# Performance work log

Hardware: AMD Instinct MI355X
Metric: run time of the kernel (lower is better)

Reference implementation:

```python
import jax, jax.numpy as jnp
import numpy as np

B, S, D, H = 2, 4096, 256, 8
P = 64               # proj_dim_l
R = S // P           # proj_dim_r = 64, P*R == S
DH = D // H          # head_dim = 32


def setup_inputs() -> dict:
    key = jax.random.key(0)
    kx, kl, kr, kv, ko = jax.random.split(key, 5)
    scale = 0.05  # stand-in for xavier-uniform scale
    x  = jax.random.normal(kx, (B, S, D), dtype=jnp.float32)
    Wl = jax.random.normal(kl, (D, P), dtype=jnp.float32) * scale
    Wr = jax.random.normal(kr, (D, R), dtype=jnp.float32) * scale
    Wv = jax.random.normal(kv, (D, D), dtype=jnp.float32) * scale
    Wo = jax.random.normal(ko, (D, D), dtype=jnp.float32) * scale
    return {"x": x, "Wl": Wl, "Wr": Wr, "Wv": Wv, "Wo": Wo}


def reference(x, Wl, Wr, Wv, Wo):
    b, s, d = x.shape
    # value projection + head split -> (b, H, S, DH). Dropout p=0 (eval) = identity.
    v = (x @ Wv).reshape(b, s, H, DH).transpose(0, 2, 1, 3)
    # factorized score: row n is vec(outer(l_n, r_n)) of length P*R == S
    l = x @ Wl                                   # (b, S, P)
    r = x @ Wr                                   # (b, S, R)
    attn = (l[:, :, :, None] * r[:, :, None, :]).reshape(b, s, s)  # (b, S, S)
    score = jax.nn.softmax(attn, axis=-1)        # (b, S, S)
    # shared score across heads, per-head value matmul
    o = jnp.einsum('bnm,bhmd->bhnd', score, v)   # (b, H, S, DH)
    o = o.transpose(0, 2, 1, 3).reshape(b, s, d) # concat heads
    return o @ Wo
```

## Files before the change

kernel.cpp:

```cpp
#include <hip/hip_runtime.h>
#include <hip/hip_bf16.h>

typedef __attribute__((ext_vector_type(8))) __bf16 bf16x8;
typedef __attribute__((ext_vector_type(4))) __bf16 bf16x4;
typedef __attribute__((ext_vector_type(4))) float  f32x4;

#define MFMA16(a, b, c) __builtin_amdgcn_mfma_f32_16x16x32_bf16((a), (b), (c), 0, 0, 0)

static constexpr size_t OFF_WVT  = 0;
static constexpr size_t OFF_WLT  = OFF_WVT + 256 * 256 * 2;
static constexpr size_t OFF_WRT  = OFF_WLT + 64 * 256 * 2;
static constexpr size_t OFF_WOT  = OFF_WRT + 64 * 256 * 2;
static constexpr size_t OFF_VT   = 1u << 20;
static constexpr size_t OFF_L    = 6u << 20;
static constexpr size_t OFF_R    = 8u << 20;
static constexpr size_t OFF_PART = 10u << 20;
static constexpr size_t OFF_ZP   = 26u << 20;

__device__ __forceinline__ float fast_exp2(float x) {
  float e;
  asm("v_exp_f32 %0, %1" : "=v"(e) : "v"(x));
  return e;
}

__device__ __forceinline__ bf16x8 cvt8(float4 a, float4 b) {
  bf16x8 o;
  o[0] = (__bf16)a.x; o[1] = (__bf16)a.y; o[2] = (__bf16)a.z; o[3] = (__bf16)a.w;
  o[4] = (__bf16)b.x; o[5] = (__bf16)b.y; o[6] = (__bf16)b.z; o[7] = (__bf16)b.w;
  return o;
}

__global__ __launch_bounds__(256) void k_prepw(const float* __restrict__ Wv,
                                               const float* __restrict__ Wl,
                                               const float* __restrict__ Wr,
                                               const float* __restrict__ Wo,
                                               __bf16* __restrict__ Wvt,
                                               __bf16* __restrict__ Wlt,
                                               __bf16* __restrict__ Wrt,
                                               __bf16* __restrict__ Wot) {
  const int idx = blockIdx.x * 256 + threadIdx.x;
  if (idx < 65536) {
    const int k = idx >> 8, n = idx & 255;
    Wvt[n * 256 + k] = (__bf16)Wv[idx];
  } else if (idx < 81920) {
    const int j = idx - 65536;
    const int k = j >> 6, n = j & 63;
    Wlt[n * 256 + k] = (__bf16)Wl[j];
  } else if (idx < 98304) {
    const int j = idx - 81920;
    const int k = j >> 6, n = j & 63;
    Wrt[n * 256 + k] = (__bf16)Wr[j];
  } else {
    const int j = idx - 98304;
    const int k = j >> 8, n = j & 255;
    Wot[n * 256 + k] = (__bf16)Wo[j];
  }
}

__global__ __launch_bounds__(256) void k_proj(const float* __restrict__ x,
                                              const __bf16* __restrict__ Wvt,
                                              const __bf16* __restrict__ Wlt,
                                              const __bf16* __restrict__ Wrt,
                                              __bf16* __restrict__ Vt,
                                              float* __restrict__ lbuf,
                                              float* __restrict__ rbuf) {
  __shared__ __align__(16) __bf16 vs[8 * 64 * 8];
  const int t = threadIdx.x;
  const int lane = t & 63, wave = t >> 6;
  const int l16 = lane & 15, quad = lane >> 4;
  const int wr = wave >> 1, wc = wave & 1;
  const int rbk = blockIdx.x;
  const int ct  = blockIdx.y;
  const __bf16* Wt;
  int colbase;
  if (ct < 4)       { Wt = Wvt; colbase = ct * 64; }
  else if (ct == 4) { Wt = Wlt; colbase = 0; }
  else              { Wt = Wrt; colbase = 0; }
  const int row0 = rbk * 64 + wr * 32;
  const int c0   = colbase + wc * 32;
  f32x4 acc[2][2] = {};
  for (int kk = 0; kk < 256; kk += 32) {
    const int ko = kk + quad * 8;
    const float* xr0 = x + (size_t)(row0 + l16) * 256 + ko;
    const float* xr1 = x + (size_t)(row0 + 16 + l16) * 256 + ko;
    bf16x8 a0 = cvt8(*(const float4*)xr0, *(const float4*)(xr0 + 4));
    bf16x8 a1 = cvt8(*(const float4*)xr1, *(const float4*)(xr1 + 4));
    bf16x8 b0 = *(const bf16x8*)(Wt + (size_t)(c0 + l16) * 256 + ko);
    bf16x8 b1 = *(const bf16x8*)(Wt + (size_t)(c0 + 16 + l16) * 256 + ko);
    acc[0][0] = MFMA16(a0, b0, acc[0][0]);
    acc[0][1] = MFMA16(a0, b1, acc[0][1]);
    acc[1][0] = MFMA16(a1, b0, acc[1][0]);
    acc[1][1] = MFMA16(a1, b1, acc[1][1]);
  }
  if (ct < 4) {
#pragma unroll
    for (int mt = 0; mt < 2; ++mt)
#pragma unroll
      for (int nt = 0; nt < 2; ++nt) {
        const int m8 = wr * 4 + mt * 2 + (quad >> 1);
        const int d  = wc * 32 + nt * 16 + l16;
        bf16x4 o;
        o.x = (__bf16)acc[mt][nt][0];
        o.y = (__bf16)acc[mt][nt][1];
        o.z = (__bf16)acc[mt][nt][2];
        o.w = (__bf16)acc[mt][nt][3];
        *(bf16x4*)(&vs[m8 * 512 + d * 8 + (quad & 1) * 4]) = o;
      }
    __syncthreads();
    const int m8 = t >> 5, s32 = t & 31;
    const int bat = rbk >> 6, mc = rbk & 63;
    bf16x8 a = *(const bf16x8*)(&vs[m8 * 512 + s32 * 16]);
    bf16x8 b = *(const bf16x8*)(&vs[m8 * 512 + s32 * 16 + 8]);
    __bf16* dst = Vt + (size_t)bat * 1048576 + (size_t)mc * 16384 +
                  m8 * 2048 + ct * 512 + s32 * 16;
    *(bf16x8*)dst       = a;
    *(bf16x8*)(dst + 8) = b;
  } else {
    float* dstb = (ct == 4) ? lbuf : rbuf;
#pragma unroll
    for (int mt = 0; mt < 2; ++mt)
#pragma unroll
      for (int nt = 0; nt < 2; ++nt) {
        const int col = c0 + nt * 16 + l16;
        const int gr  = rbk * 64 + wr * 32 + mt * 16 + quad * 4;
#pragma unroll
        for (int rr = 0; rr < 4; ++rr)
          dstb[(size_t)(gr + rr) * 64 + col] = acc[mt][nt][rr];
      }
  }
}

__global__ __launch_bounds__(512, 2) void k_attn(const float* __restrict__ lbuf,
                                                 const float* __restrict__ rbuf,
                                                 const __bf16* __restrict__ Vt,
                                                 __bf16* __restrict__ part,
                                                 float* __restrict__ zpart) {
  __shared__ __align__(16) char smem[74240];
  __bf16* vt0 = (__bf16*)smem;
  __bf16* vt1 = (__bf16*)(smem + 32768);
  float*  ls  = (float*)(smem + 65536);
  const int t = threadIdx.x;
  const int lane = t & 63, w = t >> 6;
  const int l16 = lane & 15, quad = lane >> 4;
  const int wr = w >> 1, wc = w & 1;
  const int rb = blockIdx.x;
  const int sp = blockIdx.y;
  const int g0 = rb * 128;
  const int bat = rb >> 5;
  const __bf16* Vbase = Vt + (size_t)bat * 1048576;
  const int ck0 = sp * 16;

  {
    const int idx = t * 4;
    const int row = idx >> 4, c = idx & 15;
    f32x4 v = *(const f32x4*)(lbuf + (size_t)(g0 + row) * 64 + ck0 + c);
    ls[row * 17 + c + 0] = v[0];
    ls[row * 17 + c + 1] = v[1];
    ls[row * 17 + c + 2] = v[2];
    ls[row * 17 + c + 3] = v[3];
  }
  const float LOG2E = 1.44269504088896f;
  float rreg[2][16];
#pragma unroll
  for (int mt = 0; mt < 2; ++mt) {
    const float* rp = rbuf + (size_t)(g0 + wr * 32 + mt * 16 + l16) * 64;
    f32x4 a = *(const f32x4*)(rp + quad * 8);
    f32x4 b = *(const f32x4*)(rp + quad * 8 + 4);
    f32x4 c = *(const f32x4*)(rp + 32 + quad * 8);
    f32x4 d = *(const f32x4*)(rp + 32 + quad * 8 + 4);
#pragma unroll
    for (int j = 0; j < 4; ++j) {
      rreg[mt][j]      = a[j] * LOG2E;
      rreg[mt][4 + j]  = b[j] * LOG2E;
      rreg[mt][8 + j]  = c[j] * LOG2E;
      rreg[mt][12 + j] = d[j] * LOG2E;
    }
  }

  f32x4 acc[2][8] = {};
  float zacc[2] = {0.f, 0.f};
  bf16x8 stg[4];

  {
    const __bf16* src = Vbase + (size_t)ck0 * 16384;
#pragma unroll
    for (int i = 0; i < 4; ++i) stg[i] = *(const bf16x8*)(src + (size_t)(i * 512 + t) * 8);
#pragma unroll
    for (int i = 0; i < 4; ++i) *(bf16x8*)(vt0 + (i * 512 + t) * 8) = stg[i];
  }
  __syncthreads();

  for (int kc = 0; kc < 16; ++kc) {
    __bf16* cur = (kc & 1) ? vt1 : vt0;
    __bf16* nxt = (kc & 1) ? vt0 : vt1;
    if (kc < 15) {
      const __bf16* src = Vbase + (size_t)(ck0 + kc + 1) * 16384;
#pragma unroll
      for (int i = 0; i < 4; ++i) stg[i] = *(const bf16x8*)(src + (size_t)(i * 512 + t) * 8);
    }
    bf16x8 af[2][2];
#pragma unroll
    for (int mt = 0; mt < 2; ++mt) {
      const float lv = ls[(wr * 32 + mt * 16 + l16) * 17 + kc];
#pragma unroll
      for (int kk = 0; kk < 2; ++kk)
#pragma unroll
        for (int j = 0; j < 8; ++j) {
          const float e = fast_exp2(lv * rreg[mt][kk * 8 + j]);
          zacc[mt] += e;
          af[mt][kk][j] = (__bf16)e;
        }
    }
#pragma unroll
    for (int kk = 0; kk < 2; ++kk)
#pragma unroll
      for (int nt = 0; nt < 8; ++nt) {
        bf16x8 bv = *(const bf16x8*)(cur + (kk * 4 + quad) * 2048 +
                                     (wc * 128 + nt * 16 + l16) * 8);
        acc[0][nt] = MFMA16(af[0][kk], bv, acc[0][nt]);
        acc[1][nt] = MFMA16(af[1][kk], bv, acc[1][nt]);
      }
    if (kc < 15) {
#pragma unroll
      for (int i = 0; i < 4; ++i) *(bf16x8*)(nxt + (i * 512 + t) * 8) = stg[i];
    }
    __syncthreads();
  }

#pragma unroll
  for (int mt = 0; mt < 2; ++mt) {
    float z = zacc[mt];
    z += __shfl_xor(z, 16);
    z += __shfl_xor(z, 32);
    if (wc == 0 && quad == 0)
      zpart[(size_t)sp * 8192 + g0 + wr * 32 + mt * 16 + l16] = z;
  }

  __bf16* ctile = (__bf16*)smem;
#pragma unroll
  for (int mt = 0; mt < 2; ++mt)
#pragma unroll
    for (int nt = 0; nt < 8; ++nt) {
      const int r0 = wr * 32 + mt * 16 + quad * 4;
      const int c  = wc * 128 + nt * 16 + l16;
#pragma unroll
      for (int rr = 0; rr < 4; ++rr)
        ctile[(r0 + rr) * 264 + c] = (__bf16)acc[mt][nt][rr];
    }
  __syncthreads();
  __bf16* pb = part + (size_t)sp * (8192 * 256);
#pragma unroll
  for (int p = 0; p < 8; ++p) {
    const int u = p * 512 + t;
    const int row = u >> 5, seg = u & 31;
    *(bf16x8*)(pb + (size_t)(g0 + row) * 256 + seg * 8) =
        *(const bf16x8*)(ctile + row * 264 + seg * 8);
  }
}

__global__ __launch_bounds__(256) void k_outfix(const __bf16* __restrict__ part,
                                                const float* __restrict__ zpart,
                                                const __bf16* __restrict__ Wot,
                                                float* __restrict__ out) {
  const int t = threadIdx.x;
  const int lane = t & 63, w = t >> 6;
  const int l16 = lane & 15, quad = lane >> 4;
  const int wr = w >> 1, wc = w & 1;
  const int rb = blockIdx.x;
  const int arow = rb * 32 + wr * 16 + l16;
  float z = 0.f;
#pragma unroll
  for (int s = 0; s < 4; ++s) z += zpart[(size_t)s * 8192 + arow];
  const float iz = 1.0f / z;
  f32x4 acc[8] = {};
#pragma unroll 2
  for (int ks = 0; ks < 8; ++ks) {
    const int k0 = ks * 32 + quad * 8;
    float sum[8] = {};
#pragma unroll
    for (int s = 0; s < 4; ++s) {
      bf16x8 p = *(const bf16x8*)(part + (size_t)s * (8192 * 256) + (size_t)arow * 256 + k0);
#pragma unroll
      for (int j = 0; j < 8; ++j) sum[j] += (float)p[j];
    }
    bf16x8 afr;
#pragma unroll
    for (int j = 0; j < 8; ++j) afr[j] = (__bf16)(sum[j] * iz);
#pragma unroll
    for (int nt = 0; nt < 8; ++nt) {
      bf16x8 bv = *(const bf16x8*)(Wot + (size_t)(wc * 128 + nt * 16 + l16) * 256 + k0);
      acc[nt] = MFMA16(afr, bv, acc[nt]);
    }
  }
#pragma unroll
  for (int nt = 0; nt < 8; ++nt) {
    const int col = wc * 128 + nt * 16 + l16;
    const int r0  = rb * 32 + wr * 16 + quad * 4;
#pragma unroll
    for (int rr = 0; rr < 4; ++rr)
      out[(size_t)(r0 + rr) * 256 + col] = acc[nt][rr];
  }
}

extern "C" void kernel_launch(void* const* d_in, const int* in_sizes, int n_in,
                              void* d_out, int out_size, void* d_ws, size_t ws_size,
                              hipStream_t stream) {
  const float* x  = (const float*)d_in[0];
  const float* Wl = (const float*)d_in[1];
  const float* Wr = (const float*)d_in[2];
  const float* Wv = (const float*)d_in[3];
  const float* Wo = (const float*)d_in[4];
  char* ws = (char*)d_ws;
  __bf16* Wvt = (__bf16*)(ws + OFF_WVT);
  __bf16* Wlt = (__bf16*)(ws + OFF_WLT);
  __bf16* Wrt = (__bf16*)(ws + OFF_WRT);
  __bf16* Wot = (__bf16*)(ws + OFF_WOT);
  __bf16* Vt  = (__bf16*)(ws + OFF_VT);
  float*  lb  = (float*)(ws + OFF_L);
  float*  rbf = (float*)(ws + OFF_R);
  __bf16* prt = (__bf16*)(ws + OFF_PART);
  float*  zp  = (float*)(ws + OFF_ZP);
  float*  out = (float*)d_out;

  k_prepw<<<640, 256, 0, stream>>>(Wv, Wl, Wr, Wo, Wvt, Wlt, Wrt, Wot);
  k_proj<<<dim3(128, 6), 256, 0, stream>>>(x, Wvt, Wlt, Wrt, Vt, lb, rbf);
  k_attn<<<dim3(64, 4), 512, 0, stream>>>(lb, rbf, Vt, prt, zp);
  k_outfix<<<256, 256, 0, stream>>>(prt, zp, Wot, out);
}
```

Before: 135.2 us.

## Fold Wo into Wv weights and stage V tiles with direct global-to-LDS loads

Precomputes Wv·Wo in the weight-prep kernel, using the fact that the per-head value and output projections are linear and the shared softmax commutes with them. The final kernel then becomes a simple normalize-and-sum of partials, with no MFMA output GEMM. The attention kernel's V double-buffer now uses global_load_lds instead of register staging followed by LDS stores. The folded weight product runs as a scalar fp32 loop in prep, and the fused weights are quantized to bf16 once, which changes rounding.

```diff
diff --git a/kernel.cpp b/kernel.cpp
--- a/kernel.cpp
+++ b/kernel.cpp
@@ -10,7 +10,6 @@
 static constexpr size_t OFF_WVT  = 0;
 static constexpr size_t OFF_WLT  = OFF_WVT + 256 * 256 * 2;
 static constexpr size_t OFF_WRT  = OFF_WLT + 64 * 256 * 2;
-static constexpr size_t OFF_WOT  = OFF_WRT + 64 * 256 * 2;
 static constexpr size_t OFF_VT   = 1u << 20;
 static constexpr size_t OFF_L    = 6u << 20;
 static constexpr size_t OFF_R    = 8u << 20;
@@ -28,6 +27,12 @@
   o[0] = (__bf16)a.x; o[1] = (__bf16)a.y; o[2] = (__bf16)a.z; o[3] = (__bf16)a.w;
   o[4] = (__bf16)b.x; o[5] = (__bf16)b.y; o[6] = (__bf16)b.z; o[7] = (__bf16)b.w;
   return o;
+}
+
+__device__ __forceinline__ void gll16(const __bf16* g, __bf16* l) {
+  __builtin_amdgcn_global_load_lds((const __attribute__((address_space(1))) void*)g,
+                                   (__attribute__((address_space(3))) void*)l,
+                                   16, 0, 0);
 }
 
 __global__ __launch_bounds__(256) void k_prepw(const float* __restrict__ Wv,
@@ -36,24 +41,32 @@
                                                const float* __restrict__ Wo,
                                                __bf16* __restrict__ Wvt,
                                                __bf16* __restrict__ Wlt,
-                                               __bf16* __restrict__ Wrt,
-                                               __bf16* __restrict__ Wot) {
-  const int idx = blockIdx.x * 256 + threadIdx.x;
-  if (idx < 65536) {
-    const int k = idx >> 8, n = idx & 255;
-    Wvt[n * 256 + k] = (__bf16)Wv[idx];
-  } else if (idx < 81920) {
-    const int j = idx - 65536;
-    const int k = j >> 6, n = j & 63;
-    Wlt[n * 256 + k] = (__bf16)Wl[j];
-  } else if (idx < 98304) {
-    const int j = idx - 81920;
-    const int k = j >> 6, n = j & 63;
-    Wrt[n * 256 + k] = (__bf16)Wr[j];
+                                               __bf16* __restrict__ Wrt) {
+  const int blk = blockIdx.x;
+  const int t = threadIdx.x;
+  if (blk < 128) {
+    const int idx = blk * 256 + t;
+    if (idx < 16384) {
+      const int k = idx >> 6, n = idx & 63;
+      Wlt[n * 256 + k] = (__bf16)Wl[idx];
+    } else {
+      const int j = idx - 16384;
+      const int k = j >> 6, n = j & 63;
+      Wrt[n * 256 + k] = (__bf16)Wr[j];
+    }
   } else {
-    const int j = idx - 98304;
-    const int k = j >> 8, n = j & 255;
-    Wot[n * 256 + k] = (__bf16)Wo[j];
+    const int k = blk - 128;
+    const int n = t;
+    const float* wvr = Wv + (size_t)k * 256;
+    float a0 = 0.f, a1 = 0.f, a2 = 0.f, a3 = 0.f;
+#pragma unroll 4
+    for (int j = 0; j < 256; j += 4) {
+      a0 += wvr[j + 0] * Wo[(size_t)(j + 0) * 256 + n];
+      a1 += wvr[j + 1] * Wo[(size_t)(j + 1) * 256 + n];
+      a2 += wvr[j + 2] * Wo[(size_t)(j + 2) * 256 + n];
+      a3 += wvr[j + 3] * Wo[(size_t)(j + 3) * 256 + n];
+    }
+    Wvt[(size_t)n * 256 + k] = (__bf16)((a0 + a1) + (a2 + a3));
   }
 }
 
@@ -179,14 +192,12 @@
 
   f32x4 acc[2][8] = {};
   float zacc[2] = {0.f, 0.f};
-  bf16x8 stg[4];
 
   {
     const __bf16* src = Vbase + (size_t)ck0 * 16384;
 #pragma unroll
-    for (int i = 0; i < 4; ++i) stg[i] = *(const bf16x8*)(src + (size_t)(i * 512 + t) * 8);
-#pragma unroll
-    for (int i = 0; i < 4; ++i) *(bf16x8*)(vt0 + (i * 512 + t) * 8) = stg[i];
+    for (int i = 0; i < 4; ++i)
+      gll16(src + (size_t)(i * 512 + t) * 8, vt0 + (i * 512 + (w << 6)) * 8);
   }
   __syncthreads();
 
@@ -196,7 +207,8 @@
     if (kc < 15) {
       const __bf16* src = Vbase + (size_t)(ck0 + kc + 1) * 16384;
 #pragma unroll
-      for (int i = 0; i < 4; ++i) stg[i] = *(const bf16x8*)(src + (size_t)(i * 512 + t) * 8);
+      for (int i = 0; i < 4; ++i)
+        gll16(src + (size_t)(i * 512 + t) * 8, nxt + (i * 512 + (w << 6)) * 8);
     }
     bf16x8 af[2][2];
 #pragma unroll
@@ -220,10 +232,6 @@
         acc[0][nt] = MFMA16(af[0][kk], bv, acc[0][nt]);
         acc[1][nt] = MFMA16(af[1][kk], bv, acc[1][nt]);
       }
-    if (kc < 15) {
-#pragma unroll
-      for (int i = 0; i < 4; ++i) *(bf16x8*)(nxt + (i * 512 + t) * 8) = stg[i];
-    }
     __syncthreads();
   }
 
@@ -258,48 +266,28 @@
   }
 }
 
-__global__ __launch_bounds__(256) void k_outfix(const __bf16* __restrict__ part,
-                                                const float* __restrict__ zpart,
-                                                const __bf16* __restrict__ Wot,
-                                                float* __restrict__ out) {
-  const int t = threadIdx.x;
-  const int lane = t & 63, w = t >> 6;
-  const int l16 = lane & 15, quad = lane >> 4;
-  const int wr = w >> 1, wc = w & 1;
-  const int rb = blockIdx.x;
-  const int arow = rb * 32 + wr * 16 + l16;
+__global__ __launch_bounds__(256) void k_fix(const __bf16* __restrict__ part,
+                                             const float* __restrict__ zpart,
+                                             float* __restrict__ out) {
+  const int idx = blockIdx.x * 256 + threadIdx.x;
+  const int g = idx >> 5, seg = idx & 31;
   float z = 0.f;
 #pragma unroll
-  for (int s = 0; s < 4; ++s) z += zpart[(size_t)s * 8192 + arow];
+  for (int s = 0; s < 4; ++s) z += zpart[(size_t)s * 8192 + g];
   const float iz = 1.0f / z;
-  f32x4 acc[8] = {};
-#pragma unroll 2
-  for (int ks = 0; ks < 8; ++ks) {
-    const int k0 = ks * 32 + quad * 8;
-    float sum[8] = {};
-#pragma unroll
-    for (int s = 0; s < 4; ++s) {
-      bf16x8 p = *(const bf16x8*)(part + (size_t)s * (8192 * 256) + (size_t)arow * 256 + k0);
-#pragma unroll
-      for (int j = 0; j < 8; ++j) sum[j] += (float)p[j];
-    }
-    bf16x8 afr;
-#pragma unroll
-    for (int j = 0; j < 8; ++j) afr[j] = (__bf16)(sum[j] * iz);
-#pragma unroll
-    for (int nt = 0; nt < 8; ++nt) {
-      bf16x8 bv = *(const bf16x8*)(Wot + (size_t)(wc * 128 + nt * 16 + l16) * 256 + k0);
-      acc[nt] = MFMA16(afr, bv, acc[nt]);
-    }
-  }
-#pragma unroll
-  for (int nt = 0; nt < 8; ++nt) {
-    const int col = wc * 128 + nt * 16 + l16;
-    const int r0  = rb * 32 + wr * 16 + quad * 4;
-#pragma unroll
-    for (int rr = 0; rr < 4; ++rr)
-      out[(size_t)(r0 + rr) * 256 + col] = acc[nt][rr];
-  }
+  float sum[8] = {};
+#pragma unroll
+  for (int s = 0; s < 4; ++s) {
+    bf16x8 p = *(const bf16x8*)(part + (size_t)s * (8192 * 256) + (size_t)g * 256 + seg * 8);
+#pragma unroll
+    for (int j = 0; j < 8; ++j) sum[j] += (float)p[j];
+  }
+  f32x4 o0, o1;
+#pragma unroll
+  for (int j = 0; j < 4; ++j) { o0[j] = sum[j] * iz; o1[j] = sum[4 + j] * iz; }
+  float* dst = out + (size_t)g * 256 + seg * 8;
+  *(f32x4*)dst       = o0;
+  *(f32x4*)(dst + 4) = o1;
 }
 
 extern "C" void kernel_launch(void* const* d_in, const int* in_sizes, int n_in,
@@ -314,7 +302,6 @@
   __bf16* Wvt = (__bf16*)(ws + OFF_WVT);
   __bf16* Wlt = (__bf16*)(ws + OFF_WLT);
   __bf16* Wrt = (__bf16*)(ws + OFF_WRT);
-  __bf16* Wot = (__bf16*)(ws + OFF_WOT);
   __bf16* Vt  = (__bf16*)(ws + OFF_VT);
   float*  lb  = (float*)(ws + OFF_L);
   float*  rbf = (float*)(ws + OFF_R);
@@ -322,8 +309,8 @@
   float*  zp  = (float*)(ws + OFF_ZP);
   float*  out = (float*)d_out;
 
-  k_prepw<<<640, 256, 0, stream>>>(Wv, Wl, Wr, Wo, Wvt, Wlt, Wrt, Wot);
+  k_prepw<<<384, 256, 0, stream>>>(Wv, Wl, Wr, Wo, Wvt, Wlt, Wrt);
   k_proj<<<dim3(128, 6), 256, 0, stream>>>(x, Wvt, Wlt, Wrt, Vt, lb, rbf);
   k_attn<<<dim3(64, 4), 512, 0, stream>>>(lb, rbf, Vt, prt, zp);
-  k_outfix<<<256, 256, 0, stream>>>(prt, zp, Wot, out);
-}
+  k_fix<<<1024, 256, 0, stream>>>(prt, zp, out);
+}
```

Result: faster. 122.2 us (-9.6%).
